# Kernel tuning notes

Hardware: AMD Instinct MI355X
Metric: run time of the kernel (lower is better)

Reference implementation:

```python
import jax, jax.numpy as jnp
import numpy as np

EPS = 1e-5
B, N, NPOINT, K = 16, 4096, 1024, 32
IN_CH, OUT_CH = 64, 64


def index_points(points, idx):
    # points: [B, N, C], idx: [B, ...] -> [B, ..., C]
    b = points.shape[0]
    flat = idx.reshape(b, -1)
    out = jnp.take_along_axis(points, flat[:, :, None], axis=1)
    return out.reshape(idx.shape + (points.shape[-1],))


def bn2d(x, gamma, beta):
    # x: [B, C, H, W], batch-stat BN (training mode), biased variance
    m = x.mean(axis=(0, 2, 3), keepdims=True)
    v = x.var(axis=(0, 2, 3), keepdims=True)
    return gamma[None, :, None, None] * (x - m) / jnp.sqrt(v + EPS) + beta[None, :, None, None]


def bn1d(x, gamma, beta):
    # x: [B, C, L]
    m = x.mean(axis=(0, 2), keepdims=True)
    v = x.var(axis=(0, 2), keepdims=True)
    return gamma[None, :, None] * (x - m) / jnp.sqrt(v + EPS) + beta[None, :, None]


def conv1x1(x, w, b):
    # x: [B, C, H, W], w: [O, C], b: [O]
    return jnp.einsum('bchw,oc->bohw', x, w) + b[None, :, None, None]


def setup_inputs() -> dict:
    key = jax.random.key(0)
    ks = jax.random.split(key, 16)
    inp = {
        'xyz': jax.random.normal(ks[0], (B, N, 3), jnp.float32),
        'points': jax.random.normal(ks[1], (B, N, 61), jnp.float32),
        'local_coordinates': jax.random.normal(ks[2], (B, NPOINT * K, 3), jnp.float32),
        'neighbor_lists': jax.random.randint(ks[3], (B, NPOINT, K), 0, N),
        'data_idx': jax.random.randint(ks[4], (B, NPOINT), 0, N),
        # WeightNet: 3 -> 16 -> 16 -> OUT_CH, each conv1x1 + BN2d + relu
        'w0': jax.random.normal(ks[5], (16, 3), jnp.float32) * 0.1,
        'b0': jnp.zeros((16,), jnp.float32),
        'g0': jnp.ones((16,), jnp.float32),
        'be0': jnp.zeros((16,), jnp.float32),
        'w1': jax.random.normal(ks[6], (16, 16), jnp.float32) * 0.1,
        'b1': jnp.zeros((16,), jnp.float32),
        'g1': jnp.ones((16,), jnp.float32),
        'be1': jnp.zeros((16,), jnp.float32),
        'w2': jax.random.normal(ks[7], (OUT_CH, 16), jnp.float32) * 0.1,
        'b2': jnp.zeros((OUT_CH,), jnp.float32),
        'g2': jnp.ones((OUT_CH,), jnp.float32),
        'be2': jnp.zeros((OUT_CH,), jnp.float32),
        # bn_conv over IN_CH*OUT_CH channels
        'gc': jnp.ones((IN_CH * OUT_CH,), jnp.float32),
        'bc': jnp.zeros((IN_CH * OUT_CH,), jnp.float32),
        # linear IN_CH*OUT_CH -> OUT_CH
        'lw': jax.random.normal(ks[8], (IN_CH * OUT_CH, OUT_CH), jnp.float32) * 0.01,
        'lb': jnp.zeros((OUT_CH,), jnp.float32),
        # bn_linear
        'gl': jnp.ones((OUT_CH,), jnp.float32),
        'bl': jnp.zeros((OUT_CH,), jnp.float32),
    }
    return inp


def reference(xyz, points, local_coordinates, neighbor_lists, data_idx,
              w0, b0, g0, be0, w1, b1, g1, be1, w2, b2, g2, be2,
              gc, bc, lw, lb, gl, bl):
    new_xyz = index_points(xyz, data_idx)                       # [B, NPOINT, 3]
    pts = jnp.concatenate([points, xyz], axis=2)                # [B, N, IN_CH]
    grouped = index_points(pts, neighbor_lists)                 # [B, NPOINT, K, IN_CH]
    grouped = grouped.transpose(0, 1, 3, 2)                     # [B, NPOINT, IN_CH, K]

    # WeightNet on local coordinates
    lc = local_coordinates.reshape(B, NPOINT, K, 3).transpose(0, 3, 2, 1)  # [B, 3, K, NPOINT]
    h = jax.nn.relu(bn2d(conv1x1(lc, w0, b0), g0, be0))
    h = jax.nn.relu(bn2d(conv1x1(h, w1, b1), g1, be1))
    h = jax.nn.relu(bn2d(conv1x1(h, w2, b2), g2, be2))          # [B, OUT_CH, K, NPOINT]
    weights = h.transpose(0, 3, 2, 1)                            # [B, NPOINT, K, OUT_CH]

    # aggregate over neighbors: [B, NPOINT, IN_CH, OUT_CH]
    new_points = jnp.einsum('bnik,bnko->bnio', grouped, weights)
    new_points = new_points.reshape(B, NPOINT, IN_CH * OUT_CH)

    new_points = jax.nn.relu(
        bn1d(new_points.transpose(0, 2, 1), gc, bc).transpose(0, 2, 1))
    new_points = new_points @ lw + lb                            # [B, NPOINT, OUT_CH]
    new_points = bn1d(new_points.transpose(0, 2, 1), gl, bl).transpose(0, 2, 1)
    new_points = jax.nn.relu(new_points)
    return (new_xyz, new_points)
```

## Files before the change

kernel.cpp:

```cpp
#include <hip/hip_runtime.h>
#include <hip/hip_bf16.h>

#define BB 16
#define NN 4096
#define NPOINTS 1024
#define KK 32
#define NPTS (BB*NPOINTS)
#define NWN  (BB*NPOINTS*KK)
#define EPSF 1e-5f
#define SGBLK 512
#define SGIT  4

typedef unsigned short u16;
typedef u16  u16x8 __attribute__((ext_vector_type(8)));
typedef u16  u16x4 __attribute__((ext_vector_type(4)));
typedef short s16x8 __attribute__((ext_vector_type(8)));
typedef float f32x4 __attribute__((ext_vector_type(4)));
typedef float f32x4u __attribute__((ext_vector_type(4), aligned(4)));

__device__ __forceinline__ float bf(u16 u){
  union { unsigned int i; float f; } v; v.i = ((unsigned int)u) << 16; return v.f;
}
__device__ __forceinline__ u16 f2b(float f){
  __hip_bfloat16 h = __float2bfloat16(f);
  union { __hip_bfloat16 hh; u16 u; } v; v.hh = h; return v.u;
}


__global__ __launch_bounds__(256) void k_init(const float* xyz, const int* didx, float* out,
                                              const float* lw, u16* lwbt,
                                              const float* points, u16* ptsw){
  int t = threadIdx.x;
  if (blockIdx.x < 64){
    int p = blockIdx.x * 256 + t;
    int b = p >> 10;
    int idx = didx[p];
    const float* src = xyz + ((size_t)(b * NN + idx)) * 3;
    float* dst = out + (size_t)p * 3;
    dst[0] = src[0]; dst[1] = src[1]; dst[2] = src[2];
  } else if (blockIdx.x < 128){
    __shared__ float T[64][65];
    int ib = blockIdx.x - 64;
    int kb = ib * 64;
    {
      int k = t >> 2, c4 = t & 3;
      #pragma unroll
      for (int j = 0; j < 4; ++j)
        *(f32x4*)&T[k][c4*16 + j*4] = *(const f32x4*)(lw + (size_t)(kb + k)*64 + c4*16 + j*4);
    }
    __syncthreads();
    {
      int n = t >> 2, k4 = t & 3;
      #pragma unroll
      for (int j = 0; j < 16; ++j){
        int k = k4*16 + j;
        lwbt[(size_t)n*4096 + k*64 + ib] = f2b(T[k][n]);
      }
    }
  } else {
    int gid0 = (blockIdx.x - 128) * 256 + t;
    #pragma unroll
    for (int rep = 0; rep < 4; ++rep){
      int idx = gid0 + rep * 131072;
      int row = idx >> 3, c8 = idx & 7;
      const float* prow = points + (size_t)row * 61;
      u16x8 g;
      if (c8 < 7){
        f32x4 lo = *(const f32x4u*)(prow + c8*8);
        f32x4 hi = *(const f32x4u*)(prow + c8*8 + 4);
        g[0]=f2b(lo.x); g[1]=f2b(lo.y); g[2]=f2b(lo.z); g[3]=f2b(lo.w);
        g[4]=f2b(hi.x); g[5]=f2b(hi.y); g[6]=f2b(hi.z); g[7]=f2b(hi.w);
      } else {
        const float* xr = xyz + (size_t)row * 3;
        f32x4 lo = *(const f32x4u*)(prow + 56);
        g[0]=f2b(lo.x); g[1]=f2b(lo.y); g[2]=f2b(lo.z); g[3]=f2b(lo.w);
        g[4]=f2b(prow[60]);
        g[5]=f2b(xr[0]); g[6]=f2b(xr[1]); g[7]=f2b(xr[2]);
      }
      *(u16x8*)(ptsw + (size_t)row*64 + c8*8) = g;
    }
  }
}

__global__ __launch_bounds__(256) void k_stat0(const float* lc, float* PA){
  int t = threadIdx.x;
  float a[9];
  #pragma unroll
  for (int r = 0; r < 9; ++r) a[r] = 0.f;
  size_t base = (size_t)blockIdx.x * 1024 + t;
  for (int ip = 0; ip < 4; ++ip){
    size_t p = base + (size_t)ip * 256;
    float x0 = lc[p*3], x1 = lc[p*3+1], x2 = lc[p*3+2];
    a[0]+=x0; a[1]+=x1; a[2]+=x2;
    a[3]+=x0*x0; a[4]+=x0*x1; a[5]+=x0*x2;
    a[6]+=x1*x1; a[7]+=x1*x2; a[8]+=x2*x2;
  }
  #pragma unroll
  for (int m = 1; m < 64; m <<= 1){
    #pragma unroll
    for (int r = 0; r < 9; ++r) a[r] += __shfl_xor(a[r], m);
  }
  if ((t & 63) == 0){
    float* dst = PA + (size_t)(blockIdx.x*4 + (t>>6)) * 16;
    f32x4 v0 = {a[0],a[1],a[2],a[3]}, v1 = {a[4],a[5],a[6],a[7]}, v2 = {a[8],0.f,0.f,0.f};
    *(f32x4*)dst = v0; *(f32x4*)(dst+4) = v1; *(f32x4*)(dst+8) = v2;
  }
}

__global__ __launch_bounds__(256) void k_red0(const float* PA, const float* w0, const float* b0,
                                              const float* g0, const float* be0, float* F){
  __shared__ float ms[12];
  __shared__ float a0sh[16];
  int t = threadIdx.x;
  if (t < 12){
    float s0=0,s1=0,s2=0,s3=0;
    const float* p = PA + t;
    for (int r = 0; r < 2048; r += 4){
      s0 += p[(size_t)(r+0)*16]; s1 += p[(size_t)(r+1)*16];
      s2 += p[(size_t)(r+2)*16]; s3 += p[(size_t)(r+3)*16];
    }
    ms[t] = (s0+s1)+(s2+s3);
  }
  __syncthreads();
  if (t < 16){
    float wx = w0[t*3], wy = w0[t*3+1], wz = w0[t*3+2], bb = b0[t];
    float lin = wx*ms[0] + wy*ms[1] + wz*ms[2];
    float quad = wx*wx*ms[3] + wy*wy*ms[6] + wz*wz*ms[8]
               + 2.f*(wx*wy*ms[4] + wx*wz*ms[5] + wy*wz*ms[7]);
    float S = lin + (float)NWN * bb;
    float Q = quad + 2.f*bb*lin + (float)NWN*bb*bb;
    float m = S * (1.f/NWN);
    float v = Q * (1.f/NWN) - m*m;
    float a = g0[t] * rsqrtf(v + EPSF);
    float d = be0[t] - m*a;
    a0sh[t] = a;
    F[48+t] = a*bb + d;
  }
  __syncthreads();
  if (t < 48) F[t] = a0sh[t/3] * w0[t];
}

__global__ __launch_bounds__(256) void k_statG1(const float* lc, const float* F, float* PB){
  __shared__ f32x4 w0p[16];
  __shared__ __align__(16) u16 Ht[4][16*72];
  __shared__ float GS[4][16][17];
  __shared__ float SHs[4][16];
  int t = threadIdx.x;
  int w = t >> 6, l = t & 63;
  if (t < 16){
    f32x4 wv = {F[t*3], F[t*3+1], F[t*3+2], F[48+t]};
    w0p[t] = wv;
  }
  __syncthreads();
  f32x4 acc = {0.f,0.f,0.f,0.f};
  float sh[16];
  #pragma unroll
  for (int r = 0; r < 16; ++r) sh[r] = 0.f;
  u16* Hw = &Ht[w][0];
  for (int it = 0; it < SGIT; ++it){
    size_t p = (size_t)blockIdx.x * (SGIT*256) + (size_t)it*256 + w*64 + l;
    float x0 = lc[p*3], x1 = lc[p*3+1], x2 = lc[p*3+2];
    float h[16];
    #pragma unroll
    for (int oc = 0; oc < 16; ++oc){
      f32x4 wv = w0p[oc];
      h[oc] = fmaxf(0.f, wv.x*x0 + wv.y*x1 + wv.z*x2 + wv.w);
      sh[oc] += h[oc];
    }
    #pragma unroll
    for (int c = 0; c < 16; ++c) Hw[c*72 + l] = f2b(h[c]);
    __syncthreads();
    #pragma unroll
    for (int tt = 0; tt < 2; ++tt){
      s16x8 af = *(const s16x8*)&Hw[(l & 15)*72 + tt*32 + (l >> 4)*8];
      acc = __builtin_amdgcn_mfma_f32_16x16x32_bf16(af, af, acc, 0, 0, 0);
    }
    __syncthreads();
  }
  #pragma unroll
  for (int r = 0; r < 4; ++r)
    GS[w][(l>>4)*4 + r][l & 15] = acc[r];
  #pragma unroll
  for (int m = 1; m < 64; m <<= 1){
    #pragma unroll
    for (int r = 0; r < 16; ++r) sh[r] += __shfl_xor(sh[r], m);
  }
  if (l == 0){
    #pragma unroll
    for (int r = 0; r < 16; ++r) SHs[w][r] = sh[r];
  }
  __syncthreads();
  {
    int i = t >> 4, j = t & 15;
    float g = GS[0][i][j] + GS[1][i][j] + GS[2][i][j] + GS[3][i][j];
    PB[(size_t)blockIdx.x*272 + t] = g;
    if (t < 16)
      PB[(size_t)blockIdx.x*272 + 256 + t] = SHs[0][t]+SHs[1][t]+SHs[2][t]+SHs[3][t];
  }
}

__global__ __launch_bounds__(256) void k_statG2(const float* lc, const float* F,
                                                const u16* w1Bg, float* PB){
  __shared__ f32x4 w0p[16];
  __shared__ __align__(16) u16 Ht0[4][64*40];
  __shared__ __align__(16) u16 Ht1[4][16*72];
  __shared__ float GS[4][16][17];
  __shared__ float SHs[4][16];
  int t = threadIdx.x;
  int w = t >> 6, l = t & 63;
  if (t < 16){
    f32x4 wv = {F[t*3], F[t*3+1], F[t*3+2], F[48+t]};
    w0p[t] = wv;
  }
  s16x8 w1B = *(const s16x8*)&w1Bg[l*8];
  float b1f = F[320 + (l & 15)];
  u16* H0w = &Ht0[w][0];
  u16* H1w = &Ht1[w][0];
  {
    u16x8 z8 = {0,0,0,0,0,0,0,0};
    *(u16x8*)&H0w[l*40 + 16] = z8;
    *(u16x8*)&H0w[l*40 + 24] = z8;
  }
  __syncthreads();
  f32x4 acc = {0.f,0.f,0.f,0.f};
  float shloc = 0.f;
  for (int it = 0; it < SGIT; ++it){
    size_t p = (size_t)blockIdx.x * (SGIT*256) + (size_t)it*256 + w*64 + l;
    float x0 = lc[p*3], x1 = lc[p*3+1], x2 = lc[p*3+2];
    u16x8 p0, p1;
    #pragma unroll
    for (int oc = 0; oc < 8; ++oc){
      f32x4 wv = w0p[oc];
      p0[oc] = f2b(fmaxf(0.f, wv.x*x0 + wv.y*x1 + wv.z*x2 + wv.w));
    }
    #pragma unroll
    for (int oc = 0; oc < 8; ++oc){
      f32x4 wv = w0p[8+oc];
      p1[oc] = f2b(fmaxf(0.f, wv.x*x0 + wv.y*x1 + wv.z*x2 + wv.w));
    }
    *(u16x8*)&H0w[l*40]     = p0;
    *(u16x8*)&H0w[l*40 + 8] = p1;
    __syncthreads();
    #pragma unroll
    for (int mt = 0; mt < 4; ++mt){
      s16x8 af = *(const s16x8*)&H0w[(mt*16 + (l & 15))*40 + (l >> 4)*8];
      f32x4 c = {b1f, b1f, b1f, b1f};
      c = __builtin_amdgcn_mfma_f32_16x16x32_bf16(af, w1B, c, 0, 0, 0);
      #pragma unroll
      for (int r = 0; r < 4; ++r){
        float v = fmaxf(0.f, c[r]);
        shloc += v;
        H1w[(l & 15)*72 + mt*16 + (l >> 4)*4 + r] = f2b(v);
      }
    }
    __syncthreads();
    #pragma unroll
    for (int tt = 0; tt < 2; ++tt){
      s16x8 afg = *(const s16x8*)&H1w[(l & 15)*72 + tt*32 + (l >> 4)*8];
      acc = __builtin_amdgcn_mfma_f32_16x16x32_bf16(afg, afg, acc, 0, 0, 0);
    }
    __syncthreads();
  }
  #pragma unroll
  for (int r = 0; r < 4; ++r)
    GS[w][(l>>4)*4 + r][l & 15] = acc[r];
  shloc += __shfl_xor(shloc, 16);
  shloc += __shfl_xor(shloc, 32);
  if (l < 16) SHs[w][l] = shloc;
  __syncthreads();
  {
    int i = t >> 4, j = t & 15;
    float g = GS[0][i][j] + GS[1][i][j] + GS[2][i][j] + GS[3][i][j];
    PB[(size_t)blockIdx.x*272 + t] = g;
    if (t < 16)
      PB[(size_t)blockIdx.x*272 + 256 + t] = SHs[0][t]+SHs[1][t]+SHs[2][t]+SHs[3][t];
  }
}

__global__ __launch_bounds__(256) void k_red1(const float* PB, const float* w1, const float* b1,
                                              const float* g1, const float* be1, float* F,
                                              u16* w1Bg){
  __shared__ float red[272];
  __shared__ float a1sh[16];
  int t = threadIdx.x;
  for (int e = t; e < 272; e += 256){
    float s = 0.f;
    for (int r = 0; r < SGBLK; ++r) s += PB[(size_t)r*272 + e];
    red[e] = s;
  }
  __syncthreads();
  if (t < 16){
    float wv[16];
    #pragma unroll
    for (int ic = 0; ic < 16; ++ic) wv[ic] = w1[t*16+ic];
    float lin = 0.f;
    #pragma unroll
    for (int ic = 0; ic < 16; ++ic) lin += wv[ic]*red[256+ic];
    float quad = 0.f;
    for (int i = 0; i < 16; ++i){
      float ri = 0.f;
      #pragma unroll
      for (int j = 0; j < 16; ++j) ri += wv[j]*red[i*16+j];
      quad += wv[i]*ri;
    }
    float bb = b1[t];
    float S = lin + (float)NWN * bb;
    float Q = quad + 2.f*bb*lin + (float)NWN*bb*bb;
    float m = S * (1.f/NWN);
    float v = Q * (1.f/NWN) - m*m;
    float a = g1[t] * rsqrtf(v + EPSF);
    float d = be1[t] - m*a;
    a1sh[t] = a;
    F[320+t] = a*bb + d;
  }
  __syncthreads();
  F[64 + t] = a1sh[t >> 4] * w1[t];
  if (t < 64){
    int oc = t & 15, icb = (t >> 4) * 8;
    u16x8 fr;
    #pragma unroll
    for (int j = 0; j < 8; ++j){
      int ic = icb + j;
      fr[j] = (ic < 16) ? f2b(a1sh[oc] * w1[oc*16 + ic]) : (u16)0;
    }
    *(u16x8*)&w1Bg[t*8] = fr;
  }
}

__global__ __launch_bounds__(256) void k_red2(const float* PB, const float* w2, const float* b2,
                                              const float* g2, const float* be2, float* F,
                                              u16* w2Bg){
  __shared__ float red[272];
  __shared__ float a2sh[64];
  int t = threadIdx.x;
  for (int e = t; e < 272; e += 256){
    float s = 0.f;
    for (int r = 0; r < SGBLK; ++r) s += PB[(size_t)r*272 + e];
    red[e] = s;
  }
  __syncthreads();
  if (t < 64){
    float wv[16];
    #pragma unroll
    for (int ic = 0; ic < 16; ++ic) wv[ic] = w2[t*16+ic];
    float lin = 0.f;
    #pragma unroll
    for (int ic = 0; ic < 16; ++ic) lin += wv[ic]*red[256+ic];
    float quad = 0.f;
    for (int i = 0; i < 16; ++i){
      float ri = 0.f;
      #pragma unroll
      for (int j = 0; j < 16; ++j) ri += wv[j]*red[i*16+j];
      quad += wv[i]*ri;
    }
    float bb = b2[t];
    float S = lin + (float)NWN * bb;
    float Q = quad + 2.f*bb*lin + (float)NWN*bb*bb;
    float m = S * (1.f/NWN);
    float v = Q * (1.f/NWN) - m*m;
    float a = g2[t] * rsqrtf(v + EPSF);
    float d = be2[t] - m*a;
    a2sh[t] = a;
    F[1360+t] = a*bb + d;
  }
  __syncthreads();
  for (int i = t; i < 1024; i += 256) F[336+i] = a2sh[i >> 4] * w2[i];
  {
    int ot = t >> 6, lane = t & 63;
    int oc = ot*16 + (lane & 15), icb = ((lane >> 4)) * 8;
    u16x8 fr;
    #pragma unroll
    for (int j = 0; j < 8; ++j){
      int ic = icb + j;
      fr[j] = (ic < 16) ? f2b(a2sh[oc] * w2[oc*16 + ic]) : (u16)0;
    }
    *(u16x8*)&w2Bg[t*8] = fr;
  }
}

__global__ __launch_bounds__(256) void k_main(const float* lcg, const int* nbrg,
    const u16* ptsw, const float* F,
    const u16* w1Bg, const u16* w2Bg,
    u16* npw){
  __shared__ __align__(16) u16 Gr[64*40];
  __shared__ __align__(16) u16 Wr[64*40];
  __shared__ __align__(16) u16 H0bf[32*40];
  __shared__ __align__(16) u16 H1bf[32*40];
  __shared__ float w0c[48], b0c[16];
  int t = threadIdx.x;
  int w = t >> 6, l = t & 63;
  int point = blockIdx.x;
  int bb = point >> 10;
  s16x8 w1B = *(const s16x8*)&w1Bg[l*8];
  int otA = (w & 1)*2, otB = otA + 1;
  s16x8 w2BA = *(const s16x8*)&w2Bg[(otA*64 + l)*8];
  s16x8 w2BB = *(const s16x8*)&w2Bg[(otB*64 + l)*8];
  float b1f = F[320 + (l & 15)];
  float b2fA = F[1360 + otA*16 + (l & 15)];
  float b2fB = F[1360 + otB*16 + (l & 15)];
  if (t < 48) w0c[t] = F[t];
  if (t < 16) b0c[t] = F[48+t];
  {
    int k = t >> 3, c = 16 + (t & 7)*2;
    *(unsigned int*)&H0bf[k*40 + c] = 0u;
    *(unsigned int*)&H1bf[k*40 + c] = 0u;
  }
  {
    int kg = w*8 + (l >> 3), c8 = l & 7;
    int n = nbrg[(size_t)point*32 + kg];
    u16x8 g = *(const u16x8*)(ptsw + (size_t)(bb * NN + n)*64 + c8*8);
    int kphys = ((w ^ (c8 & 3)) << 3) + (l >> 3);
    #pragma unroll
    for (int j = 0; j < 8; ++j)
      Gr[(c8*8 + j)*40 + kphys] = g[j];
  }
  __syncthreads();
  {
    int k = t >> 3, oc0 = (t & 7)*2;
    const float* xp = lcg + (size_t)point*96 + k*3;
    float x0 = xp[0], x1 = xp[1], x2 = xp[2];
    #pragma unroll
    for (int e = 0; e < 2; ++e){
      int oc = oc0 + e;
      float y = w0c[oc*3]*x0 + w0c[oc*3+1]*x1 + w0c[oc*3+2]*x2 + b0c[oc];
      H0bf[k*40 + oc] = f2b(fmaxf(0.f, y));
    }
  }
  __syncthreads();
  if (w < 2){
    int kt = w;
    s16x8 af = *(const s16x8*)&H0bf[(kt*16 + (l & 15))*40 + (l >> 4)*8];
    f32x4 acc = {b1f, b1f, b1f, b1f};
    acc = __builtin_amdgcn_mfma_f32_16x16x32_bf16(af, w1B, acc, 0, 0, 0);
    #pragma unroll
    for (int r = 0; r < 4; ++r)
      H1bf[(kt*16 + (l >> 4)*4 + r)*40 + (l & 15)] = f2b(fmaxf(0.f, acc[r]));
  }
  __syncthreads();
  {
    int kt = w >> 1;
    s16x8 af = *(const s16x8*)&H1bf[(kt*16 + (l & 15))*40 + (l >> 4)*8];
    int kbase = kt*16 + (l >> 4)*4;
    f32x4 accA = {b2fA, b2fA, b2fA, b2fA};
    accA = __builtin_amdgcn_mfma_f32_16x16x32_bf16(af, w2BA, accA, 0, 0, 0);
    u16x4 sA;
    sA[0]=f2b(fmaxf(0.f,accA[0])); sA[1]=f2b(fmaxf(0.f,accA[1]));
    sA[2]=f2b(fmaxf(0.f,accA[2])); sA[3]=f2b(fmaxf(0.f,accA[3]));
    *(u16x4*)&Wr[(otA*16 + (l & 15))*40 + kbase] = sA;
    f32x4 accB = {b2fB, b2fB, b2fB, b2fB};
    accB = __builtin_amdgcn_mfma_f32_16x16x32_bf16(af, w2BB, accB, 0, 0, 0);
    u16x4 sB;
    sB[0]=f2b(fmaxf(0.f,accB[0])); sB[1]=f2b(fmaxf(0.f,accB[1]));
    sB[2]=f2b(fmaxf(0.f,accB[2])); sB[3]=f2b(fmaxf(0.f,accB[3]));
    *(u16x4*)&Wr[(otB*16 + (l & 15))*40 + kbase] = sB;
  }
  __syncthreads();
  {
    int li = l & 15, lkb = l >> 4, lr = (l >> 4) * 4;
    s16x8 bfrag = *(const s16x8*)&Wr[(w*16 + li)*40 + lkb*8];
    size_t obase = (size_t)point*4096 + (size_t)(w*16 + li)*64 + lr;
    #pragma unroll
    for (int it = 0; it < 4; ++it){
      int ch = it*16 + li;
      int key = (ch >> 3) & 3;
      s16x8 afrag = *(const s16x8*)&Gr[ch*40 + ((lkb ^ key) << 3)];
      f32x4 z = {0.f, 0.f, 0.f, 0.f};
      f32x4 d = __builtin_amdgcn_mfma_f32_16x16x32_bf16(afrag, bfrag, z, 0, 0, 0);
      u16x4 st;
      st[0] = f2b(d[0]); st[1] = f2b(d[1]); st[2] = f2b(d[2]); st[3] = f2b(d[3]);
      *(u16x4*)(npw + obase + it*16) = st;
    }
  }
}

__global__ __launch_bounds__(256) void k_statC(const u16* npw, float* PC){
  int t = threadIdx.x;
  float s[16], q[16];
  #pragma unroll
  for (int j = 0; j < 16; ++j){ s[j] = 0.f; q[j] = 0.f; }
  size_t rowbase = (size_t)blockIdx.x * 64;
  for (int p = 0; p < 64; ++p){
    const u16* row = npw + (rowbase + p) * 4096 + t * 16;
    u16x8 a = *(const u16x8*)row;
    u16x8 b = *(const u16x8*)(row + 8);
    #pragma unroll
    for (int j = 0; j < 8; ++j){ float v = bf(a[j]); s[j]   += v; q[j]   += v*v; }
    #pragma unroll
    for (int j = 0; j < 8; ++j){ float v = bf(b[j]); s[8+j] += v; q[8+j] += v*v; }
  }
  float* dst = PC + (size_t)blockIdx.x * 8192 + t * 16;
  #pragma unroll
  for (int j = 0; j < 16; ++j){ dst[j] = s[j]; dst[4096 + j] = q[j]; }
}

__global__ __launch_bounds__(256) void k_finC(const float* PC, const float* gc, const float* bc,
                                              float* AC, float* DC){
  int qpos = blockIdx.x * 256 + threadIdx.x;
  float s = 0.f, q = 0.f;
  for (int r = 0; r < 256; ++r){
    s += PC[(size_t)r * 8192 + qpos];
    q += PC[(size_t)r * 8192 + 4096 + qpos];
  }
  int ch = (qpos & 63)*64 + (qpos >> 6);
  float m = s * (1.f/16384.f);
  float v = q * (1.f/16384.f) - m*m;
  float a = gc[ch] * rsqrtf(v + EPSF);
  AC[qpos] = a; DC[qpos] = bc[ch] - m*a;
}

__global__ __launch_bounds__(256) void k_linear(const u16* npw, const float* AC, const float* DC,
                                                const u16* lwbt, const float* lb, float* yw,
                                                float* PL){
  __shared__ u16 Al[32*72];
  __shared__ u16 Bl[64*72];
  __shared__ float cps[64], cpq[64];
  int t = threadIdx.x;
  int w = t >> 6, l = t & 63;
  int rowbase = blockIdx.x * 32;
  int mt = w & 1, np2 = w >> 1;
  f32x4 acc0 = {0.f,0.f,0.f,0.f}, acc1 = acc0;
  for (int kb = 0; kb < 4096; kb += 64){
    __syncthreads();
    {
      int r = t >> 3, c8 = t & 7;
      int kk = kb + c8*8;
      u16x8 u = *(const u16x8*)(npw + (size_t)(rowbase + r)*4096 + kk);
      f32x4 alo = *(const f32x4*)(AC + kk), ahi = *(const f32x4*)(AC + kk + 4);
      f32x4 dlo = *(const f32x4*)(DC + kk), dhi = *(const f32x4*)(DC + kk + 4);
      u16x8 o;
      o[0] = f2b(fmaxf(0.f, alo.x*bf(u[0]) + dlo.x));
      o[1] = f2b(fmaxf(0.f, alo.y*bf(u[1]) + dlo.y));
      o[2] = f2b(fmaxf(0.f, alo.z*bf(u[2]) + dlo.z));
      o[3] = f2b(fmaxf(0.f, alo.w*bf(u[3]) + dlo.w));
      o[4] = f2b(fmaxf(0.f, ahi.x*bf(u[4]) + dhi.x));
      o[5] = f2b(fmaxf(0.f, ahi.y*bf(u[5]) + dhi.y));
      o[6] = f2b(fmaxf(0.f, ahi.z*bf(u[6]) + dhi.z));
      o[7] = f2b(fmaxf(0.f, ahi.w*bf(u[7]) + dhi.w));
      *(u16x8*)&Al[r*72 + c8*8] = o;
    }
    #pragma unroll
    for (int jj = 0; jj < 2; ++jj){
      int n = (t >> 3) + jj*32, c8 = t & 7;
      u16x8 u = *(const u16x8*)(lwbt + (size_t)n*4096 + kb + c8*8);
      *(u16x8*)&Bl[n*72 + c8*8] = u;
    }
    __syncthreads();
    #pragma unroll
    for (int ks = 0; ks < 2; ++ks){
      s16x8 af  = *(const s16x8*)&Al[(mt*16 + (l & 15))*72 + ks*32 + (l >> 4)*8];
      s16x8 bf0 = *(const s16x8*)&Bl[((np2*2    )*16 + (l & 15))*72 + ks*32 + (l >> 4)*8];
      s16x8 bf1 = *(const s16x8*)&Bl[((np2*2 + 1)*16 + (l & 15))*72 + ks*32 + (l >> 4)*8];
      acc0 = __builtin_amdgcn_mfma_f32_16x16x32_bf16(af, bf0, acc0, 0, 0, 0);
      acc1 = __builtin_amdgcn_mfma_f32_16x16x32_bf16(af, bf1, acc1, 0, 0, 0);
    }
  }
  int col0 = np2*32 + (l & 15), col1 = col0 + 16;
  float lb0 = lb[col0], lb1 = lb[col1];
  float s0 = 0.f, q0 = 0.f, s1 = 0.f, q1 = 0.f;
  if (t < 64){ cps[t] = 0.f; cpq[t] = 0.f; }
  __syncthreads();
  #pragma unroll
  for (int r = 0; r < 4; ++r){
    int row = rowbase + mt*16 + (l >> 4)*4 + r;
    float y0 = acc0[r] + lb0;
    float y1 = acc1[r] + lb1;
    yw[(size_t)row*64 + col0] = y0;
    yw[(size_t)row*64 + col1] = y1;
    s0 += y0; q0 += y0*y0; s1 += y1; q1 += y1*y1;
  }
  atomicAdd(&cps[col0], s0); atomicAdd(&cpq[col0], q0);
  atomicAdd(&cps[col1], s1); atomicAdd(&cpq[col1], q1);
  __syncthreads();
  if (t < 64){
    PL[blockIdx.x*128 + t]      = cps[t];
    PL[blockIdx.x*128 + 64 + t] = cpq[t];
  }
}

__global__ __launch_bounds__(128) void k_redF(const float* PL, float* SL){
  int t = threadIdx.x;
  float s = 0.f;
  for (int b = 0; b < 512; ++b) s += PL[b*128 + t];
  SL[t] = s;
}

__global__ __launch_bounds__(256) void k_final(const float* yw, const float* SL,
                                               const float* gl, const float* bl, float* out){
  int e = (blockIdx.x * 256 + threadIdx.x) * 4;
  int o = e & 63;
  f32x4 y = *(const f32x4*)(yw + e);
  f32x4 r;
  #pragma unroll
  for (int j = 0; j < 4; ++j){
    float m = SL[o+j] * (1.f/16384.f);
    float v = SL[64+o+j] * (1.f/16384.f) - m*m;
    float a = gl[o+j] * rsqrtf(v + EPSF);
    float d = bl[o+j] - m*a;
    r[j] = fmaxf(0.f, a*y[j] + d);
  }
  *(f32x4*)(out + 49152 + e) = r;
}

extern "C" void kernel_launch(void* const* d_in, const int* in_sizes, int n_in,
                              void* d_out, int out_size, void* d_ws, size_t ws_size,
                              hipStream_t stream){
  (void)in_sizes; (void)n_in; (void)out_size; (void)ws_size;
  const float* xyz    = (const float*)d_in[0];
  const float* points = (const float*)d_in[1];
  const float* lc     = (const float*)d_in[2];
  const int*   nbrl   = (const int*)d_in[3];
  const int*   didx   = (const int*)d_in[4];
  const float* w0 = (const float*)d_in[5];
  const float* b0 = (const float*)d_in[6];
  const float* g0 = (const float*)d_in[7];
  const float* be0= (const float*)d_in[8];
  const float* w1 = (const float*)d_in[9];
  const float* b1 = (const float*)d_in[10];
  const float* g1 = (const float*)d_in[11];
  const float* be1= (const float*)d_in[12];
  const float* w2 = (const float*)d_in[13];
  const float* b2 = (const float*)d_in[14];
  const float* g2 = (const float*)d_in[15];
  const float* be2= (const float*)d_in[16];
  const float* gc = (const float*)d_in[17];
  const float* bc = (const float*)d_in[18];
  const float* lw = (const float*)d_in[19];
  const float* lb = (const float*)d_in[20];
  const float* gl = (const float*)d_in[21];
  const float* bl = (const float*)d_in[22];
  float* out = (float*)d_out;
  char* ws = (char*)d_ws;

  float* F   = (float*)ws;
  float* SL  = F + 1536;
  float* AC  = SL + 128;
  float* DC  = AC + 4096;
  float* PA  = DC + 4096;
  float* PB1 = PA + 32768;
  float* PB2 = PB1 + 139264;
  float* PL  = PB2 + 139264;
  u16*  w1Bg = (u16*)(PL + 65536);
  u16*  w2Bg = w1Bg + 512;
  float* PC  = (float*)(ws + 4194304);
  u16*  npw  = (u16*)(ws + 4194304 + 8388608);
  float* yw  = (float*)(ws + 4194304 + 8388608 + 134217728);
  u16*  lwbt = (u16*)(ws + 4194304 + 8388608 + 134217728 + 4194304);
  u16*  ptsw = (u16*)(ws + 4194304 + 8388608 + 134217728 + 4194304 + 1048576);

  k_init  <<<640,   256, 0, stream>>>(xyz, didx, out, lw, lwbt, points, ptsw);
  k_stat0 <<<512,   256, 0, stream>>>(lc, PA);
  k_red0  <<<1,     256, 0, stream>>>(PA, w0, b0, g0, be0, F);
  k_statG1<<<SGBLK, 256, 0, stream>>>(lc, F, PB1);
  k_red1  <<<1,     256, 0, stream>>>(PB1, w1, b1, g1, be1, F, w1Bg);
  k_statG2<<<SGBLK, 256, 0, stream>>>(lc, F, w1Bg, PB2);
  k_red2  <<<1,     256, 0, stream>>>(PB2, w2, b2, g2, be2, F, w2Bg);
  k_main  <<<16384, 256, 0, stream>>>(lc, nbrl, ptsw, F, w1Bg, w2Bg, npw);
  k_statC <<<256,   256, 0, stream>>>(npw, PC);
  k_finC  <<<16,    256, 0, stream>>>(PC, gc, bc, AC, DC);
  k_linear<<<512,   256, 0, stream>>>(npw, AC, DC, lwbt, lb, yw, PL);
  k_redF  <<<1,     128, 0, stream>>>(PL, SL);
  k_final <<<1024,  256, 0, stream>>>(yw, SL, gl, bl, out);
}
```

Measured before the change: 258.7 us.

## Process two points per block in k_main to cut barriers and idle waves

k_main now handles two points per block, using double-sized shared buffers and half as many blocks. The layer-1 MFMA stage, which previously left two of four waves idle, now keeps all four waves busy across the two points. Layer-2 weights and biases stay in registers for all four output tiles, and the w0/b0 staging through shared memory along with one barrier are removed by loading layer-0 weights straight into registers. In exchange, each block uses more shared memory and more registers, which may lower occupancy.

```diff
diff --git a/kernel.cpp b/kernel.cpp
--- a/kernel.cpp
+++ b/kernel.cpp
@@ -382,93 +382,111 @@
     const u16* ptsw, const float* F,
     const u16* w1Bg, const u16* w2Bg,
     u16* npw){
-  __shared__ __align__(16) u16 Gr[64*40];
-  __shared__ __align__(16) u16 Wr[64*40];
-  __shared__ __align__(16) u16 H0bf[32*40];
-  __shared__ __align__(16) u16 H1bf[32*40];
-  __shared__ float w0c[48], b0c[16];
+  __shared__ __align__(16) u16 Gr[2][64*40];
+  __shared__ __align__(16) u16 Wr[2][64*40];
+  __shared__ __align__(16) u16 H0bf[2][32*40];
+  __shared__ __align__(16) u16 H1bf[2][32*40];
   int t = threadIdx.x;
   int w = t >> 6, l = t & 63;
-  int point = blockIdx.x;
-  int bb = point >> 10;
-  s16x8 w1B = *(const s16x8*)&w1Bg[l*8];
-  int otA = (w & 1)*2, otB = otA + 1;
-  s16x8 w2BA = *(const s16x8*)&w2Bg[(otA*64 + l)*8];
-  s16x8 w2BB = *(const s16x8*)&w2Bg[(otB*64 + l)*8];
-  float b1f = F[320 + (l & 15)];
-  float b2fA = F[1360 + otA*16 + (l & 15)];
-  float b2fB = F[1360 + otB*16 + (l & 15)];
-  if (t < 48) w0c[t] = F[t];
-  if (t < 16) b0c[t] = F[48+t];
+  int p0 = blockIdx.x * 2;
+  s16x8 w1B  = *(const s16x8*)&w1Bg[l*8];
+  s16x8 w2B0 = *(const s16x8*)&w2Bg[(0*64 + l)*8];
+  s16x8 w2B1 = *(const s16x8*)&w2Bg[(1*64 + l)*8];
+  s16x8 w2B2 = *(const s16x8*)&w2Bg[(2*64 + l)*8];
+  s16x8 w2B3 = *(const s16x8*)&w2Bg[(3*64 + l)*8];
+  float b1f  = F[320 + (l & 15)];
+  float b2f0 = F[1360 +  0 + (l & 15)];
+  float b2f1 = F[1360 + 16 + (l & 15)];
+  float b2f2 = F[1360 + 32 + (l & 15)];
+  float b2f3 = F[1360 + 48 + (l & 15)];
+  int oc0 = (t & 7) * 2;
+  f32x4 w0a = {F[oc0*3], F[oc0*3+1], F[oc0*3+2], F[48+oc0]};
+  f32x4 w0b = {F[oc0*3+3], F[oc0*3+4], F[oc0*3+5], F[48+oc0+1]};
   {
     int k = t >> 3, c = 16 + (t & 7)*2;
-    *(unsigned int*)&H0bf[k*40 + c] = 0u;
-    *(unsigned int*)&H1bf[k*40 + c] = 0u;
+    *(unsigned int*)&H0bf[0][k*40 + c] = 0u;
+    *(unsigned int*)&H0bf[1][k*40 + c] = 0u;
+    *(unsigned int*)&H1bf[0][k*40 + c] = 0u;
+    *(unsigned int*)&H1bf[1][k*40 + c] = 0u;
   }
   {
     int kg = w*8 + (l >> 3), c8 = l & 7;
-    int n = nbrg[(size_t)point*32 + kg];
-    u16x8 g = *(const u16x8*)(ptsw + (size_t)(bb * NN + n)*64 + c8*8);
     int kphys = ((w ^ (c8 & 3)) << 3) + (l >> 3);
     #pragma unroll
-    for (int j = 0; j < 8; ++j)
-      Gr[(c8*8 + j)*40 + kphys] = g[j];
-  }
-  __syncthreads();
-  {
-    int k = t >> 3, oc0 = (t & 7)*2;
-    const float* xp = lcg + (size_t)point*96 + k*3;
-    float x0 = xp[0], x1 = xp[1], x2 = xp[2];
-    #pragma unroll
-    for (int e = 0; e < 2; ++e){
-      int oc = oc0 + e;
-      float y = w0c[oc*3]*x0 + w0c[oc*3+1]*x1 + w0c[oc*3+2]*x2 + b0c[oc];
-      H0bf[k*40 + oc] = f2b(fmaxf(0.f, y));
-    }
-  }
-  __syncthreads();
-  if (w < 2){
-    int kt = w;
-    s16x8 af = *(const s16x8*)&H0bf[(kt*16 + (l & 15))*40 + (l >> 4)*8];
+    for (int pt = 0; pt < 2; ++pt){
+      int point = p0 + pt;
+      int bbp = point >> 10;
+      int n = nbrg[(size_t)point*32 + kg];
+      u16x8 g = *(const u16x8*)(ptsw + (size_t)(bbp * NN + n)*64 + c8*8);
+      #pragma unroll
+      for (int j = 0; j < 8; ++j)
+        Gr[pt][(c8*8 + j)*40 + kphys] = g[j];
+    }
+  }
+  {
+    int k = t >> 3;
+    #pragma unroll
+    for (int pt = 0; pt < 2; ++pt){
+      const float* xp = lcg + (size_t)(p0 + pt)*96 + k*3;
+      float x0 = xp[0], x1 = xp[1], x2 = xp[2];
+      H0bf[pt][k*40 + oc0]     = f2b(fmaxf(0.f, w0a.x*x0 + w0a.y*x1 + w0a.z*x2 + w0a.w));
+      H0bf[pt][k*40 + oc0 + 1] = f2b(fmaxf(0.f, w0b.x*x0 + w0b.y*x1 + w0b.z*x2 + w0b.w));
+    }
+  }
+  __syncthreads();
+  {
+    int pt = w >> 1, kt = w & 1;
+    s16x8 af = *(const s16x8*)&H0bf[pt][(kt*16 + (l & 15))*40 + (l >> 4)*8];
     f32x4 acc = {b1f, b1f, b1f, b1f};
     acc = __builtin_amdgcn_mfma_f32_16x16x32_bf16(af, w1B, acc, 0, 0, 0);
     #pragma unroll
     for (int r = 0; r < 4; ++r)
-      H1bf[(kt*16 + (l >> 4)*4 + r)*40 + (l & 15)] = f2b(fmaxf(0.f, acc[r]));
-  }
-  __syncthreads();
-  {
-    int kt = w >> 1;
-    s16x8 af = *(const s16x8*)&H1bf[(kt*16 + (l & 15))*40 + (l >> 4)*8];
+      H1bf[pt][(kt*16 + (l >> 4)*4 + r)*40 + (l & 15)] = f2b(fmaxf(0.f, acc[r]));
+  }
+  __syncthreads();
+  {
+    int pt = w & 1, kt = w >> 1;
+    s16x8 af = *(const s16x8*)&H1bf[pt][(kt*16 + (l & 15))*40 + (l >> 4)*8];
     int kbase = kt*16 + (l >> 4)*4;
-    f32x4 accA = {b2fA, b2fA, b2fA, b2fA};
-    accA = __builtin_amdgcn_mfma_f32_16x16x32_bf16(af, w2BA, accA, 0, 0, 0);
-    u16x4 sA;
-    sA[0]=f2b(fmaxf(0.f,accA[0])); sA[1]=f2b(fmaxf(0.f,accA[1]));
-    sA[2]=f2b(fmaxf(0.f,accA[2])); sA[3]=f2b(fmaxf(0.f,accA[3]));
-    *(u16x4*)&Wr[(otA*16 + (l & 15))*40 + kbase] = sA;
-    f32x4 accB = {b2fB, b2fB, b2fB, b2fB};
-    accB = __builtin_amdgcn_mfma_f32_16x16x32_bf16(af, w2BB, accB, 0, 0, 0);
-    u16x4 sB;
-    sB[0]=f2b(fmaxf(0.f,accB[0])); sB[1]=f2b(fmaxf(0.f,accB[1]));
-    sB[2]=f2b(fmaxf(0.f,accB[2])); sB[3]=f2b(fmaxf(0.f,accB[3]));
-    *(u16x4*)&Wr[(otB*16 + (l & 15))*40 + kbase] = sB;
+    f32x4 a0c = {b2f0,b2f0,b2f0,b2f0};
+    a0c = __builtin_amdgcn_mfma_f32_16x16x32_bf16(af, w2B0, a0c, 0, 0, 0);
+    u16x4 s0v; s0v[0]=f2b(fmaxf(0.f,a0c[0])); s0v[1]=f2b(fmaxf(0.f,a0c[1]));
+    s0v[2]=f2b(fmaxf(0.f,a0c[2])); s0v[3]=f2b(fmaxf(0.f,a0c[3]));
+    *(u16x4*)&Wr[pt][( 0 + (l & 15))*40 + kbase] = s0v;
+    f32x4 a1c = {b2f1,b2f1,b2f1,b2f1};
+    a1c = __builtin_amdgcn_mfma_f32_16x16x32_bf16(af, w2B1, a1c, 0, 0, 0);
+    u16x4 s1v; s1v[0]=f2b(fmaxf(0.f,a1c[0])); s1v[1]=f2b(fmaxf(0.f,a1c[1]));
+    s1v[2]=f2b(fmaxf(0.f,a1c[2])); s1v[3]=f2b(fmaxf(0.f,a1c[3]));
+    *(u16x4*)&Wr[pt][(16 + (l & 15))*40 + kbase] = s1v;
+    f32x4 a2c = {b2f2,b2f2,b2f2,b2f2};
+    a2c = __builtin_amdgcn_mfma_f32_16x16x32_bf16(af, w2B2, a2c, 0, 0, 0);
+    u16x4 s2v; s2v[0]=f2b(fmaxf(0.f,a2c[0])); s2v[1]=f2b(fmaxf(0.f,a2c[1]));
+    s2v[2]=f2b(fmaxf(0.f,a2c[2])); s2v[3]=f2b(fmaxf(0.f,a2c[3]));
+    *(u16x4*)&Wr[pt][(32 + (l & 15))*40 + kbase] = s2v;
+    f32x4 a3c = {b2f3,b2f3,b2f3,b2f3};
+    a3c = __builtin_amdgcn_mfma_f32_16x16x32_bf16(af, w2B3, a3c, 0, 0, 0);
+    u16x4 s3v; s3v[0]=f2b(fmaxf(0.f,a3c[0])); s3v[1]=f2b(fmaxf(0.f,a3c[1]));
+    s3v[2]=f2b(fmaxf(0.f,a3c[2])); s3v[3]=f2b(fmaxf(0.f,a3c[3]));
+    *(u16x4*)&Wr[pt][(48 + (l & 15))*40 + kbase] = s3v;
   }
   __syncthreads();
   {
     int li = l & 15, lkb = l >> 4, lr = (l >> 4) * 4;
-    s16x8 bfrag = *(const s16x8*)&Wr[(w*16 + li)*40 + lkb*8];
-    size_t obase = (size_t)point*4096 + (size_t)(w*16 + li)*64 + lr;
-    #pragma unroll
-    for (int it = 0; it < 4; ++it){
-      int ch = it*16 + li;
-      int key = (ch >> 3) & 3;
-      s16x8 afrag = *(const s16x8*)&Gr[ch*40 + ((lkb ^ key) << 3)];
-      f32x4 z = {0.f, 0.f, 0.f, 0.f};
-      f32x4 d = __builtin_amdgcn_mfma_f32_16x16x32_bf16(afrag, bfrag, z, 0, 0, 0);
-      u16x4 st;
-      st[0] = f2b(d[0]); st[1] = f2b(d[1]); st[2] = f2b(d[2]); st[3] = f2b(d[3]);
-      *(u16x4*)(npw + obase + it*16) = st;
+    #pragma unroll
+    for (int pt = 0; pt < 2; ++pt){
+      s16x8 bfrag = *(const s16x8*)&Wr[pt][(w*16 + li)*40 + lkb*8];
+      size_t obase = (size_t)(p0 + pt)*4096 + (size_t)(w*16 + li)*64 + lr;
+      #pragma unroll
+      for (int it = 0; it < 4; ++it){
+        int ch = it*16 + li;
+        int key = (ch >> 3) & 3;
+        s16x8 afrag = *(const s16x8*)&Gr[pt][ch*40 + ((lkb ^ key) << 3)];
+        f32x4 z = {0.f, 0.f, 0.f, 0.f};
+        f32x4 d = __builtin_amdgcn_mfma_f32_16x16x32_bf16(afrag, bfrag, z, 0, 0, 0);
+        u16x4 st;
+        st[0] = f2b(d[0]); st[1] = f2b(d[1]); st[2] = f2b(d[2]); st[3] = f2b(d[3]);
+        *(u16x4*)(npw + obase + it*16) = st;
+      }
     }
   }
 }
@@ -654,7 +672,7 @@
   k_red1  <<<1,     256, 0, stream>>>(PB1, w1, b1, g1, be1, F, w1Bg);
   k_statG2<<<SGBLK, 256, 0, stream>>>(lc, F, w1Bg, PB2);
   k_red2  <<<1,     256, 0, stream>>>(PB2, w2, b2, g2, be2, F, w2Bg);
-  k_main  <<<16384, 256, 0, stream>>>(lc, nbrl, ptsw, F, w1Bg, w2Bg, npw);
+  k_main  <<<8192,  256, 0, stream>>>(lc, nbrl, ptsw, F, w1Bg, w2Bg, npw);
   k_statC <<<256,   256, 0, stream>>>(npw, PC);
   k_finC  <<<16,    256, 0, stream>>>(PC, gc, bc, AC, DC);
   k_linear<<<512,   256, 0, stream>>>(npw, AC, DC, lwbt, lb, yw, PL);
```

After: 251.8 us. 2.7% less time.
